# Kernel optimization log

Hardware: AMD Instinct MI355X
Metric: run time of the kernel (lower is better)

Reference implementation:

```python
import jax, jax.numpy as jnp
import numpy as np

EPS_IN = 1e-5   # torch InstanceNorm2d default eps
EPS_VAR = 1e-6  # clamp floor on attention-weighted variance


def _inorm(x):
    # x: (b, c, t); InstanceNorm2d with affine=False normalizes over spatial dims
    m = x.mean(axis=-1, keepdims=True)
    v = x.var(axis=-1, keepdims=True)  # biased variance, matches torch eval-mode IN
    return (x - m) / jnp.sqrt(v + EPS_IN)


def setup_inputs() -> dict:
    key = jax.random.key(0)
    ks = jax.random.split(key, 9)
    b, t, d = 4, 4096, 256
    sc = 1.0 / np.sqrt(d).astype(np.float32)
    return {
        "fc": jax.random.normal(ks[0], (b, t, d), jnp.float32),
        "fs": jax.random.normal(ks[1], (b, t, d), jnp.float32),
        "fcs": jax.random.normal(ks[2], (b, t, d), jnp.float32),
        "Wf": jax.random.normal(ks[3], (d, d), jnp.float32) * sc,
        "bf": jax.random.normal(ks[4], (d,), jnp.float32) * 0.01,
        "Wg": jax.random.normal(ks[5], (d, d), jnp.float32) * sc,
        "bg": jax.random.normal(ks[6], (d,), jnp.float32) * 0.01,
        "Wh": jax.random.normal(ks[7], (d, d), jnp.float32) * sc,
        "bh": jax.random.normal(ks[8], (d,), jnp.float32) * 0.01,
    }


def reference(fc, fs, fcs, Wf, bf, Wg, bg, Wh, bh):
    # (b, t, d) -> channel-first flat (b, d, t); 1x1 conv == per-token linear
    fc_t = jnp.swapaxes(fc, 1, 2)
    fs_t = jnp.swapaxes(fs, 1, 2)
    fcs_t = jnp.swapaxes(fcs, 1, 2)

    Q = jnp.einsum('oc,bct->bto', Wf, _inorm(fc_t)) + bf                 # (b,t,d)
    K = jnp.einsum('oc,bct->bot', Wg, _inorm(fs_t)) + bg[None, :, None]  # (b,d,t)
    V = jnp.einsum('oc,bct->bto', Wh, fs_t) + bh                         # (b,t,d)

    A = jax.nn.softmax(jnp.einsum('btd,bdu->btu', Q, K), axis=-1)        # (b,t,t)
    M = jnp.einsum('btu,bud->btd', A, V)                                 # mean
    Var = jnp.einsum('btu,bud->btd', A, V * V) - M * M                   # E[v^2]-E[v]^2
    S = jnp.sqrt(jnp.maximum(Var, EPS_VAR))

    out_t = jnp.swapaxes(S, 1, 2) * _inorm(fcs_t) + jnp.swapaxes(M, 1, 2)  # (b,d,t)
    return jnp.swapaxes(out_t, 1, 2)  # (b, t, d)
```

## Files before the change

kernel.cpp:

```cpp
#include <hip/hip_runtime.h>
#include <math.h>

#define B 4
#define T 4096
#define D 256
#define NCH 16
#define CHT (T / NCH)
#define KC 32
#define NCHUNK (T / KC)

typedef __attribute__((ext_vector_type(8))) _Float16 half8;
typedef __attribute__((ext_vector_type(4))) _Float16 half4;
typedef __attribute__((ext_vector_type(4))) float f32x4;

__global__ __launch_bounds__(256) void k_stats_part(
    const float* __restrict__ fc, const float* __restrict__ fs,
    const float* __restrict__ fcs, float* __restrict__ part)
{
    int blk = blockIdx.x;
    int tensor = blk / (B * NCH);
    int rem = blk % (B * NCH);
    int b = rem / NCH, ch = rem % NCH;
    const float* x = (tensor == 0) ? fc : ((tensor == 1) ? fs : fcs);
    int c = threadIdx.x;
    const float* p = x + ((size_t)b * T + (size_t)ch * CHT) * D + c;
    float s = 0.f, ss = 0.f;
    for (int t = 0; t < CHT; ++t) {
        float v = p[(size_t)t * D];
        s += v; ss += v * v;
    }
    float* o = part + (((size_t)tensor * B + b) * NCH + ch) * 2 * D;
    o[c] = s;
    o[D + c] = ss;
}

__global__ __launch_bounds__(256) void k_stats_final(
    const float* __restrict__ part, float* __restrict__ stats)
{
    int blk = blockIdx.x;
    int tensor = blk / B, b = blk % B;
    int c = threadIdx.x;
    const float* pp = part + (((size_t)tensor * B + b) * NCH) * 2 * D;
    float s = 0.f, ss = 0.f;
    for (int ch = 0; ch < NCH; ++ch) {
        s  += pp[(size_t)ch * 2 * D + c];
        ss += pp[(size_t)ch * 2 * D + D + c];
    }
    float mean = s / (float)T;
    float var  = ss / (float)T - mean * mean;
    float rstd = rsqrtf(var + 1e-5f);
    float* st = stats + (size_t)tensor * 2 * B * D;
    st[(size_t)b * D + c]          = mean;
    st[(size_t)B * D + b * D + c]  = rstd;
}

__global__ __launch_bounds__(256) void k_wprep(
    const float* __restrict__ Wf, const float* __restrict__ Wg,
    const float* __restrict__ Wh, _Float16* __restrict__ Whi,
    _Float16* __restrict__ Wlo)
{
    int blk = blockIdx.x;
    int which = blk >> 8, row = blk & 255;
    const float* Wsrc = (which == 0) ? Wf : ((which == 1) ? Wg : Wh);
    int c = threadIdx.x;
    float v = Wsrc[row * 256 + c];
    _Float16 h = (_Float16)v;
    float l = v - (float)h;
    size_t off = ((size_t)which << 16) + (row << 8) + c;
    Whi[off] = h;
    Wlo[off] = (_Float16)l;
}

__global__ __launch_bounds__(256) void k_gemm_mfma(
    const float* __restrict__ x, const _Float16* __restrict__ Whi,
    const _Float16* __restrict__ Wlo, const float* __restrict__ bias,
    const float* __restrict__ stats, int use_norm, int mode,
    _Float16* __restrict__ out1,
    _Float16* __restrict__ oV, _Float16* __restrict__ oV2h,
    _Float16* __restrict__ oV2l)
{
    __shared__ _Float16 Xl[64 * 256];
    int m0 = blockIdx.x * 64;
    int b = m0 / T;
    int tid = threadIdx.x;
    const float* mean = stats;
    const float* rstd = stats + B * D;

    #pragma unroll
    for (int j = 0; j < 16; ++j) {
        int idx = tid + j * 256;
        int m = idx >> 6, c4 = idx & 63;
        float4 v = *(const float4*)(x + ((size_t)(m0 + m)) * D + c4 * 4);
        if (use_norm) {
            int c = c4 * 4;
            v.x = (v.x - mean[b * D + c + 0]) * rstd[b * D + c + 0];
            v.y = (v.y - mean[b * D + c + 1]) * rstd[b * D + c + 1];
            v.z = (v.z - mean[b * D + c + 2]) * rstd[b * D + c + 2];
            v.w = (v.w - mean[b * D + c + 3]) * rstd[b * D + c + 3];
        }
        half4 h;
        h[0] = (_Float16)v.x; h[1] = (_Float16)v.y;
        h[2] = (_Float16)v.z; h[3] = (_Float16)v.w;
        *(half4*)&Xl[m * 256 + ((c4 * 4) ^ ((m & 7) << 3))] = h;
    }
    __syncthreads();

    const int l = tid & 63, w = tid >> 6;
    const int lo16 = l & 15, hi4 = l >> 4;
    const int row = w * 16 + lo16;

    float bias_v[16];
    #pragma unroll
    for (int nt = 0; nt < 16; ++nt) bias_v[nt] = bias[nt * 16 + lo16];

    f32x4 acc[16];
    #pragma unroll
    for (int nt = 0; nt < 16; ++nt) acc[nt] = (f32x4){0.f, 0.f, 0.f, 0.f};

    #pragma unroll
    for (int kk = 0; kk < 8; ++kk) {
        half8 a = *(const half8*)&Xl[row * 256 + ((kk * 32 + hi4 * 8) ^ ((row & 7) << 3))];
        #pragma unroll
        for (int nt = 0; nt < 16; ++nt) {
            size_t wo = (size_t)(nt * 16 + lo16) * 256 + kk * 32 + hi4 * 8;
            half8 bh = *(const half8*)(Whi + wo);
            acc[nt] = __builtin_amdgcn_mfma_f32_16x16x32_f16(a, bh, acc[nt], 0, 0, 0);
            half8 bl = *(const half8*)(Wlo + wo);
            acc[nt] = __builtin_amdgcn_mfma_f32_16x16x32_f16(a, bl, acc[nt], 0, 0, 0);
        }
    }

    if (mode == 1) {
        #pragma unroll
        for (int nt = 0; nt < 16; ++nt)
            #pragma unroll
            for (int r = 0; r < 4; ++r) {
                int t = m0 + w * 16 + hi4 * 4 + r;
                out1[(size_t)t * D + nt * 16 + lo16] = (_Float16)(acc[nt][r] + bias_v[nt]);
            }
    } else {
        int t0 = (m0 % T) + w * 16 + hi4 * 4;
        #pragma unroll
        for (int nt = 0; nt < 16; ++nt) {
            int o = nt * 16 + lo16;
            half4 vh, h4, l4;
            #pragma unroll
            for (int r = 0; r < 4; ++r) {
                float v = acc[nt][r] + bias_v[nt];
                _Float16 vhh = (_Float16)v;
                float f2 = (float)vhh * (float)vhh;
                _Float16 hh = (_Float16)f2;
                float fl = f2 - (float)hh;
                vh[r] = vhh; h4[r] = hh; l4[r] = (_Float16)fl;
            }
            size_t base = ((size_t)b * D + o) * T + t0;
            *(half4*)(oV   + base) = vh;
            *(half4*)(oV2h + base) = h4;
            *(half4*)(oV2l + base) = l4;
        }
    }
}

__global__ __launch_bounds__(512, 2) void k_attn(
    const _Float16* __restrict__ Qg, const _Float16* __restrict__ Kg,
    const _Float16* __restrict__ Vtg, const _Float16* __restrict__ V2hg,
    const _Float16* __restrict__ V2lg, const float* __restrict__ fcs,
    const float* __restrict__ stats_fcs, float* __restrict__ out)
{
    __shared__ __align__(16) _Float16 Kl [2][32 * 256];
    __shared__ __align__(16) _Float16 Vl [2][256 * 32];
    __shared__ __align__(16) _Float16 V2h[2][256 * 32];
    __shared__ __align__(16) _Float16 V2l[2][256 * 32];
    __shared__ __align__(16) _Float16 Pl[64 * 32];
    __shared__ float corr_lds[64];
    __shared__ float l_lds[64];
    __shared__ int   flags[4];

    const int tid = threadIdx.x;
    const int l = tid & 63;
    const int w = tid >> 6;
    const int b  = blockIdx.x >> 6;
    const int q0 = (blockIdx.x & 63) << 6;
    const int lo16 = l & 15, hi4 = l >> 4;

    const _Float16* KgB  = Kg   + (size_t)b * T * D;
    const _Float16* VtB  = Vtg  + (size_t)b * D * T;
    const _Float16* V2hB = V2hg + (size_t)b * D * T;
    const _Float16* V2lB = V2lg + (size_t)b * D * T;

    half8 qf[8];
    if (w < 4) {
        const _Float16* qp = Qg + ((size_t)(b * T + q0 + 16 * w + lo16)) * D + hi4 * 8;
        #pragma unroll
        for (int kk = 0; kk < 8; ++kk) qf[kk] = *(const half8*)(qp + kk * 32);
    }

    f32x4 accM[4][2], accE[4][2];
    #pragma unroll
    for (int qs = 0; qs < 4; ++qs)
        #pragma unroll
        for (int jj = 0; jj < 2; ++jj) {
            accM[qs][jj] = (f32x4){0.f, 0.f, 0.f, 0.f};
            accE[qs][jj] = (f32x4){0.f, 0.f, 0.f, 0.f};
        }
    float m_run[4] = {-1e9f, -1e9f, -1e9f, -1e9f};
    float lv[4] = {0.f, 0.f, 0.f, 0.f};

    auto stage = [&](int kcs, int cb) {
        int k0 = kcs * KC;
        int t2 = tid & 255;
        half8 kr[4], vr[4], vhr[4], vlr[4];
        #pragma unroll
        for (int i = 0; i < 4; ++i) {
            int g = t2 + i * 256;
            kr[i] = *(const half8*)(KgB + (size_t)(k0 + (g >> 5)) * D + (g & 31) * 8);
        }
        #pragma unroll
        for (int i = 0; i < 4; ++i) {
            int g = t2 + i * 256; int d = g >> 2, kg = g & 3;
            size_t off = (size_t)d * T + k0 + kg * 8;
            vr[i]  = *(const half8*)(VtB  + off);
            vhr[i] = *(const half8*)(V2hB + off);
            vlr[i] = *(const half8*)(V2lB + off);
        }
        #pragma unroll
        for (int i = 0; i < 4; ++i) {
            int g = t2 + i * 256; int rr = g >> 5, cg = g & 31;
            *(half8*)&Kl[cb][rr * 256 + ((cg ^ (rr & 7)) << 3)] = kr[i];
        }
        #pragma unroll
        for (int i = 0; i < 4; ++i) {
            int g = t2 + i * 256; int d = g >> 2, kg = g & 3;
            int p = d * 32 + ((kg ^ ((d >> 1) & 3)) << 3);
            *(half8*)&Vl[cb][p]  = vr[i];
            *(half8*)&V2h[cb][p] = vhr[i];
            *(half8*)&V2l[cb][p] = vlr[i];
        }
    };

    if (w >= 4) stage(0, 0);
    __syncthreads();
    int cur = 0;

    for (int kc = 0; kc < NCHUNK; ++kc) {
        if (w < 4) {
            f32x4 c0 = (f32x4){0.f, 0.f, 0.f, 0.f}, c1 = (f32x4){0.f, 0.f, 0.f, 0.f};
            #pragma unroll
            for (int kk = 0; kk < 8; ++kk) {
                int cg = kk * 4 + hi4;
                half8 b0 = *(const half8*)&Kl[cur][lo16 * 256 + ((cg ^ (lo16 & 7)) << 3)];
                half8 b1 = *(const half8*)&Kl[cur][(16 + lo16) * 256 + ((cg ^ ((16 + lo16) & 7)) << 3)];
                c0 = __builtin_amdgcn_mfma_f32_16x16x32_f16(qf[kk], b0, c0, 0, 0, 0);
                c1 = __builtin_amdgcn_mfma_f32_16x16x32_f16(qf[kk], b1, c1, 0, 0, 0);
            }

            float cm[4];
            #pragma unroll
            for (int r = 0; r < 4; ++r) cm[r] = fmaxf(c0[r], c1[r]);
            float tmax = fmaxf(fmaxf(cm[0] - m_run[0], cm[1] - m_run[1]),
                               fmaxf(cm[2] - m_run[2], cm[3] - m_run[3]));
            int flagv = 0;
            if (__any(tmax > 10.f)) {
                flagv = 1;
                float corr[4];
                #pragma unroll
                for (int r = 0; r < 4; ++r) {
                    float rm = cm[r];
                    rm = fmaxf(rm, __shfl_xor(rm, 1));
                    rm = fmaxf(rm, __shfl_xor(rm, 2));
                    rm = fmaxf(rm, __shfl_xor(rm, 4));
                    rm = fmaxf(rm, __shfl_xor(rm, 8));
                    float mn = fmaxf(m_run[r], rm);
                    corr[r] = __expf(m_run[r] - mn);
                    m_run[r] = mn;
                    lv[r] *= corr[r];
                }
                if (lo16 == 0) {
                    #pragma unroll
                    for (int r = 0; r < 4; ++r)
                        corr_lds[w * 16 + hi4 * 4 + r] = corr[r];
                }
            }
            if (l == 0) flags[w] = flagv;

            float p0[4], p1[4];
            #pragma unroll
            for (int r = 0; r < 4; ++r) {
                p0[r] = __expf(c0[r] - m_run[r]);
                p1[r] = __expf(c1[r] - m_run[r]);
                lv[r] += p0[r] + p1[r];
            }
            #pragma unroll
            for (int r = 0; r < 4; ++r) {
                int q = 16 * w + hi4 * 4 + r;
                int ka = lo16, kb = 16 + lo16;
                Pl[q * 32 + (((ka >> 3) ^ (q & 3)) << 3) + (ka & 7)] = (_Float16)p0[r];
                Pl[q * 32 + (((kb >> 3) ^ (q & 3)) << 3) + (kb & 7)] = (_Float16)p1[r];
            }
        } else {
            if (kc + 1 < NCHUNK) stage(kc + 1, cur ^ 1);
        }
        __syncthreads();

        #pragma unroll
        for (int qs = 0; qs < 4; ++qs) {
            if (flags[qs]) {
                #pragma unroll
                for (int r = 0; r < 4; ++r) {
                    float c = corr_lds[qs * 16 + hi4 * 4 + r];
                    accM[qs][0][r] *= c; accM[qs][1][r] *= c;
                    accE[qs][0][r] *= c; accE[qs][1][r] *= c;
                }
            }
        }

        half8 pa[4];
        #pragma unroll
        for (int qs = 0; qs < 4; ++qs) {
            int q = qs * 16 + lo16;
            pa[qs] = *(const half8*)&Pl[q * 32 + ((hi4 ^ (q & 3)) << 3)];
        }

        #pragma unroll
        for (int jj = 0; jj < 2; ++jj) {
            int d = (2 * w + jj) * 16 + lo16;
            int p = d * 32 + ((hi4 ^ ((d >> 1) & 3)) << 3);
            half8 bh  = *(const half8*)&Vl[cur][p];
            half8 b2h = *(const half8*)&V2h[cur][p];
            half8 b2l = *(const half8*)&V2l[cur][p];
            #pragma unroll
            for (int qs = 0; qs < 4; ++qs) {
                accM[qs][jj] = __builtin_amdgcn_mfma_f32_16x16x32_f16(pa[qs], bh,  accM[qs][jj], 0, 0, 0);
                accE[qs][jj] = __builtin_amdgcn_mfma_f32_16x16x32_f16(pa[qs], b2h, accE[qs][jj], 0, 0, 0);
                accE[qs][jj] = __builtin_amdgcn_mfma_f32_16x16x32_f16(pa[qs], b2l, accE[qs][jj], 0, 0, 0);
            }
        }

        __syncthreads();
        cur ^= 1;
    }

    if (w < 4) {
        #pragma unroll
        for (int r = 0; r < 4; ++r) {
            float lr = lv[r];
            lr += __shfl_xor(lr, 1);
            lr += __shfl_xor(lr, 2);
            lr += __shfl_xor(lr, 4);
            lr += __shfl_xor(lr, 8);
            if (lo16 == 0) l_lds[w * 16 + hi4 * 4 + r] = lr;
        }
    }
    __syncthreads();

    const float* mfc = stats_fcs;
    const float* rfc = stats_fcs + B * D;
    #pragma unroll
    for (int qs = 0; qs < 4; ++qs) {
        #pragma unroll
        for (int r = 0; r < 4; ++r) {
            float linv = 1.f / l_lds[qs * 16 + hi4 * 4 + r];
            int q = q0 + qs * 16 + hi4 * 4 + r;
            size_t rowb = ((size_t)(b * T + q)) * D;
            #pragma unroll
            for (int jj = 0; jj < 2; ++jj) {
                int d = (2 * w + jj) * 16 + lo16;
                float M  = accM[qs][jj][r] * linv;
                float E2 = accE[qs][jj][r] * linv;
                float S  = sqrtf(fmaxf(E2 - M * M, 1e-6f));
                float f  = fcs[rowb + d];
                out[rowb + d] = S * ((f - mfc[b * D + d]) * rfc[b * D + d]) + M;
            }
        }
    }
}

extern "C" void kernel_launch(void* const* d_in, const int* in_sizes, int n_in,
                              void* d_out, int out_size, void* d_ws, size_t ws_size,
                              hipStream_t stream)
{
    const float* fc  = (const float*)d_in[0];
    const float* fs  = (const float*)d_in[1];
    const float* fcs = (const float*)d_in[2];
    const float* Wf  = (const float*)d_in[3];
    const float* bf  = (const float*)d_in[4];
    const float* Wg  = (const float*)d_in[5];
    const float* bg  = (const float*)d_in[6];
    const float* Wh  = (const float*)d_in[7];
    const float* bh  = (const float*)d_in[8];
    float* out = (float*)d_out;

    char* ws = (char*)d_ws;
    float* stats = (float*)ws;
    float* part  = (float*)(ws + (64 << 10));
    _Float16* Whi = (_Float16*)(ws + (512 << 10));
    _Float16* Wlo = Whi + 3 * 65536;
    _Float16* Qg   = (_Float16*)(ws + (2 << 20));
    _Float16* Kg   = Qg  + (size_t)B * T * D;
    _Float16* Vtg  = Kg  + (size_t)B * T * D;
    _Float16* V2hg = Vtg + (size_t)B * T * D;
    _Float16* V2lg = V2hg + (size_t)B * T * D;

    k_stats_part<<<3 * B * NCH, 256, 0, stream>>>(fc, fs, fcs, part);
    k_stats_final<<<3 * B, 256, 0, stream>>>(part, stats);
    k_wprep<<<3 * 256, 256, 0, stream>>>(Wf, Wg, Wh, Whi, Wlo);

    float* st_fc  = stats + 0 * 2 * B * D;
    float* st_fs  = stats + 1 * 2 * B * D;
    float* st_fcs = stats + 2 * 2 * B * D;

    k_gemm_mfma<<<(B * T) / 64, 256, 0, stream>>>(fc, Whi,             Wlo,             bf, st_fc, 1, 1, Qg, nullptr, nullptr, nullptr);
    k_gemm_mfma<<<(B * T) / 64, 256, 0, stream>>>(fs, Whi + 65536,     Wlo + 65536,     bg, st_fs, 1, 1, Kg, nullptr, nullptr, nullptr);
    k_gemm_mfma<<<(B * T) / 64, 256, 0, stream>>>(fs, Whi + 2 * 65536, Wlo + 2 * 65536, bh, st_fs, 0, 2, nullptr, Vtg, V2hg, V2lg);

    k_attn<<<B * (T / 64), 512, 0, stream>>>(Qg, Kg, Vtg, V2hg, V2lg, fcs, st_fcs, out);
}
```

Baseline: 366.2 us.

## Merge prep and projection launches, swizzle attention blocks, add MFMA priority hints

Folds the weight hi/lo split into the stats-partial kernel and merges the three projection GEMMs into one launch, cutting the launch count from seven to four. The attention kernel's block index is remapped so consecutive blocks spread across batches and query tiles, and s_setprio raises wave priority around the MFMA loops. Launch bounds on attention drop from 2 to 1 blocks per SM, which lets the compiler use more registers but may lower occupancy.

Result: faster. 356.2 us (-2.7%).

```diff
diff --git a/kernel.cpp b/kernel.cpp
--- a/kernel.cpp
+++ b/kernel.cpp
@@ -13,25 +13,43 @@
 typedef __attribute__((ext_vector_type(4))) _Float16 half4;
 typedef __attribute__((ext_vector_type(4))) float f32x4;
 
-__global__ __launch_bounds__(256) void k_stats_part(
+__global__ __launch_bounds__(256) void k_prep(
     const float* __restrict__ fc, const float* __restrict__ fs,
-    const float* __restrict__ fcs, float* __restrict__ part)
+    const float* __restrict__ fcs, float* __restrict__ part,
+    const float* __restrict__ Wf, const float* __restrict__ Wg,
+    const float* __restrict__ Wh, _Float16* __restrict__ Whi,
+    _Float16* __restrict__ Wlo)
 {
     int blk = blockIdx.x;
-    int tensor = blk / (B * NCH);
-    int rem = blk % (B * NCH);
-    int b = rem / NCH, ch = rem % NCH;
-    const float* x = (tensor == 0) ? fc : ((tensor == 1) ? fs : fcs);
-    int c = threadIdx.x;
-    const float* p = x + ((size_t)b * T + (size_t)ch * CHT) * D + c;
-    float s = 0.f, ss = 0.f;
-    for (int t = 0; t < CHT; ++t) {
-        float v = p[(size_t)t * D];
-        s += v; ss += v * v;
-    }
-    float* o = part + (((size_t)tensor * B + b) * NCH + ch) * 2 * D;
-    o[c] = s;
-    o[D + c] = ss;
+    if (blk < 192) {
+        int tensor = blk / (B * NCH);
+        int rem = blk % (B * NCH);
+        int b = rem / NCH, ch = rem % NCH;
+        const float* x = (tensor == 0) ? fc : ((tensor == 1) ? fs : fcs);
+        int c = threadIdx.x;
+        const float* p = x + ((size_t)b * T + (size_t)ch * CHT) * D + c;
+        float s = 0.f, ss = 0.f;
+        for (int t = 0; t < CHT; ++t) {
+            float v = p[(size_t)t * D];
+            s += v; ss += v * v;
+        }
+        float* o = part + (((size_t)tensor * B + b) * NCH + ch) * 2 * D;
+        o[c] = s;
+        o[D + c] = ss;
+    } else {
+        int base = (blk - 192) * 2048;
+        #pragma unroll
+        for (int i = 0; i < 8; ++i) {
+            int idx = base + threadIdx.x + i * 256;
+            int which = idx >> 16, rc = idx & 65535;
+            const float* Wsrc = (which == 0) ? Wf : ((which == 1) ? Wg : Wh);
+            float v = Wsrc[rc];
+            _Float16 h = (_Float16)v;
+            float l = v - (float)h;
+            Whi[idx] = h;
+            Wlo[idx] = (_Float16)l;
+        }
+    }
 }
 
 __global__ __launch_bounds__(256) void k_stats_final(
@@ -54,37 +72,27 @@
     st[(size_t)B * D + b * D + c]  = rstd;
 }
 
-__global__ __launch_bounds__(256) void k_wprep(
-    const float* __restrict__ Wf, const float* __restrict__ Wg,
-    const float* __restrict__ Wh, _Float16* __restrict__ Whi,
-    _Float16* __restrict__ Wlo)
-{
-    int blk = blockIdx.x;
-    int which = blk >> 8, row = blk & 255;
-    const float* Wsrc = (which == 0) ? Wf : ((which == 1) ? Wg : Wh);
-    int c = threadIdx.x;
-    float v = Wsrc[row * 256 + c];
-    _Float16 h = (_Float16)v;
-    float l = v - (float)h;
-    size_t off = ((size_t)which << 16) + (row << 8) + c;
-    Whi[off] = h;
-    Wlo[off] = (_Float16)l;
-}
-
-__global__ __launch_bounds__(256) void k_gemm_mfma(
-    const float* __restrict__ x, const _Float16* __restrict__ Whi,
-    const _Float16* __restrict__ Wlo, const float* __restrict__ bias,
-    const float* __restrict__ stats, int use_norm, int mode,
-    _Float16* __restrict__ out1,
+__global__ __launch_bounds__(256) void k_gemm3(
+    const float* __restrict__ fc, const float* __restrict__ fs,
+    const _Float16* __restrict__ Whi, const _Float16* __restrict__ Wlo,
+    const float* __restrict__ bf, const float* __restrict__ bg,
+    const float* __restrict__ bh, const float* __restrict__ stats,
+    _Float16* __restrict__ Qg, _Float16* __restrict__ Kg,
     _Float16* __restrict__ oV, _Float16* __restrict__ oV2h,
     _Float16* __restrict__ oV2l)
 {
     __shared__ _Float16 Xl[64 * 256];
-    int m0 = blockIdx.x * 64;
-    int b = m0 / T;
-    int tid = threadIdx.x;
-    const float* mean = stats;
-    const float* rstd = stats + B * D;
+    const int which = blockIdx.x >> 8;
+    const int m0 = (blockIdx.x & 255) * 64;
+    const int b = m0 / T;
+    const int tid = threadIdx.x;
+    const float* x = (which == 0) ? fc : fs;
+    const float* bias = (which == 0) ? bf : ((which == 1) ? bg : bh);
+    const _Float16* Wh_ = Whi + which * 65536;
+    const _Float16* Wl_ = Wlo + which * 65536;
+    const int use_norm = (which != 2);
+    const float* mean = stats + (which == 0 ? 0 : 1) * 2 * B * D;
+    const float* rstd = mean + B * D;
 
     #pragma unroll
     for (int j = 0; j < 16; ++j) {
@@ -123,14 +131,15 @@
         #pragma unroll
         for (int nt = 0; nt < 16; ++nt) {
             size_t wo = (size_t)(nt * 16 + lo16) * 256 + kk * 32 + hi4 * 8;
-            half8 bh = *(const half8*)(Whi + wo);
-            acc[nt] = __builtin_amdgcn_mfma_f32_16x16x32_f16(a, bh, acc[nt], 0, 0, 0);
-            half8 bl = *(const half8*)(Wlo + wo);
-            acc[nt] = __builtin_amdgcn_mfma_f32_16x16x32_f16(a, bl, acc[nt], 0, 0, 0);
-        }
-    }
-
-    if (mode == 1) {
+            half8 bhf = *(const half8*)(Wh_ + wo);
+            acc[nt] = __builtin_amdgcn_mfma_f32_16x16x32_f16(a, bhf, acc[nt], 0, 0, 0);
+            half8 blf = *(const half8*)(Wl_ + wo);
+            acc[nt] = __builtin_amdgcn_mfma_f32_16x16x32_f16(a, blf, acc[nt], 0, 0, 0);
+        }
+    }
+
+    if (which != 2) {
+        _Float16* out1 = (which == 0) ? Qg : Kg;
         #pragma unroll
         for (int nt = 0; nt < 16; ++nt)
             #pragma unroll
@@ -161,7 +170,7 @@
     }
 }
 
-__global__ __launch_bounds__(512, 2) void k_attn(
+__global__ __launch_bounds__(512, 1) void k_attn(
     const _Float16* __restrict__ Qg, const _Float16* __restrict__ Kg,
     const _Float16* __restrict__ Vtg, const _Float16* __restrict__ V2hg,
     const _Float16* __restrict__ V2lg, const float* __restrict__ fcs,
@@ -179,8 +188,9 @@
     const int tid = threadIdx.x;
     const int l = tid & 63;
     const int w = tid >> 6;
-    const int b  = blockIdx.x >> 6;
-    const int q0 = (blockIdx.x & 63) << 6;
+    const int swz = (blockIdx.x & 7) * 32 + (blockIdx.x >> 3);
+    const int b  = swz >> 6;
+    const int q0 = (swz & 63) << 6;
     const int lo16 = l & 15, hi4 = l >> 4;
 
     const _Float16* KgB  = Kg   + (size_t)b * T * D;
@@ -245,6 +255,7 @@
     for (int kc = 0; kc < NCHUNK; ++kc) {
         if (w < 4) {
             f32x4 c0 = (f32x4){0.f, 0.f, 0.f, 0.f}, c1 = (f32x4){0.f, 0.f, 0.f, 0.f};
+            __builtin_amdgcn_s_setprio(1);
             #pragma unroll
             for (int kk = 0; kk < 8; ++kk) {
                 int cg = kk * 4 + hi4;
@@ -253,6 +264,7 @@
                 c0 = __builtin_amdgcn_mfma_f32_16x16x32_f16(qf[kk], b0, c0, 0, 0, 0);
                 c1 = __builtin_amdgcn_mfma_f32_16x16x32_f16(qf[kk], b1, c1, 0, 0, 0);
             }
+            __builtin_amdgcn_s_setprio(0);
 
             float cm[4];
             #pragma unroll
@@ -321,6 +333,7 @@
             pa[qs] = *(const half8*)&Pl[q * 32 + ((hi4 ^ (q & 3)) << 3)];
         }
 
+        __builtin_amdgcn_s_setprio(1);
         #pragma unroll
         for (int jj = 0; jj < 2; ++jj) {
             int d = (2 * w + jj) * 16 + lo16;
@@ -335,6 +348,7 @@
                 accE[qs][jj] = __builtin_amdgcn_mfma_f32_16x16x32_f16(pa[qs], b2l, accE[qs][jj], 0, 0, 0);
             }
         }
+        __builtin_amdgcn_s_setprio(0);
 
         __syncthreads();
         cur ^= 1;
@@ -401,17 +415,13 @@
     _Float16* V2hg = Vtg + (size_t)B * T * D;
     _Float16* V2lg = V2hg + (size_t)B * T * D;
 
-    k_stats_part<<<3 * B * NCH, 256, 0, stream>>>(fc, fs, fcs, part);
+    k_prep<<<288, 256, 0, stream>>>(fc, fs, fcs, part, Wf, Wg, Wh, Whi, Wlo);
     k_stats_final<<<3 * B, 256, 0, stream>>>(part, stats);
-    k_wprep<<<3 * 256, 256, 0, stream>>>(Wf, Wg, Wh, Whi, Wlo);
-
-    float* st_fc  = stats + 0 * 2 * B * D;
-    float* st_fs  = stats + 1 * 2 * B * D;
+
     float* st_fcs = stats + 2 * 2 * B * D;
 
-    k_gemm_mfma<<<(B * T) / 64, 256, 0, stream>>>(fc, Whi,             Wlo,             bf, st_fc, 1, 1, Qg, nullptr, nullptr, nullptr);
-    k_gemm_mfma<<<(B * T) / 64, 256, 0, stream>>>(fs, Whi + 65536,     Wlo + 65536,     bg, st_fs, 1, 1, Kg, nullptr, nullptr, nullptr);
-    k_gemm_mfma<<<(B * T) / 64, 256, 0, stream>>>(fs, Whi + 2 * 65536, Wlo + 2 * 65536, bh, st_fs, 0, 2, nullptr, Vtg, V2hg, V2lg);
+    k_gemm3<<<3 * 256, 256, 0, stream>>>(fc, fs, Whi, Wlo, bf, bg, bh, stats,
+                                         Qg, Kg, Vtg, V2hg, V2lg);
 
     k_attn<<<B * (T / 64), 512, 0, stream>>>(Qg, Kg, Vtg, V2hg, V2lg, fcs, st_fcs, out);
 }
```
